# Kernel tuning notes

Hardware: AMD Instinct MI355X
Metric: run time of the kernel (lower is better)

The kernel has to match this reference:

```python
import jax, jax.numpy as jnp
import numpy as np

N = 100000   # nodes
E = 800000   # edges
F = 64       # num_features == hidden_dim
D = 64       # hidden_dim
L = 3        # num_gc_layers
NG = 512     # num graphs in batch
BN_EPS = 1e-5


def setup_inputs() -> dict:
    key = jax.random.key(0)
    ks = jax.random.split(key, 16)
    s = 0.05
    return {
        "x": jax.random.normal(ks[0], (N, F), jnp.float32),
        "edge_index": jax.random.randint(ks[1], (2, E), 0, N),
        "batch": jnp.sort(jax.random.randint(ks[2], (N,), 0, NG)),
        "W1": jax.random.normal(ks[3], (L, F, D), jnp.float32) * s,
        "b1": jnp.zeros((L, D), jnp.float32),
        "W2": jax.random.normal(ks[4], (L, D, D), jnp.float32) * s,
        "b2": jnp.zeros((L, D), jnp.float32),
        "gin_eps": jnp.zeros((L,), jnp.float32),
        "gin_bias": jnp.zeros((L, D), jnp.float32),
        "bn_gamma": jnp.ones((L, D), jnp.float32),
        "bn_beta": jnp.zeros((L, D), jnp.float32),
        "Wp1": jax.random.normal(ks[5], (L * D, L * D), jnp.float32) * s,
        "bp1": jnp.zeros((L * D,), jnp.float32),
        "Wp2": jax.random.normal(ks[6], (L * D, L * D), jnp.float32) * s,
        "bp2": jnp.zeros((L * D,), jnp.float32),
    }


def reference(x, edge_index, batch, W1, b1, W2, b2, gin_eps, gin_bias,
              bn_gamma, bn_beta, Wp1, bp1, Wp2, bp2):
    row, col = edge_index[0], edge_index[1]
    h = x
    xs = []
    for i in range(L):
        # sparse adj @ h : sum over incoming edges (adj[row, col] = 1)
        agg = jax.ops.segment_sum(h[col], row, num_segments=N)
        z = (1.0 + gin_eps[i]) * h + agg
        # GIN internal MLP: Linear -> ReLU -> Linear -> ReLU
        z = jax.nn.relu(z @ W1[i] + b1[i])
        z = jax.nn.relu(z @ W2[i] + b2[i])
        # conv bias + relu (outer F.relu in Encoder is idempotent)
        z = jax.nn.relu(z + gin_bias[i])
        # BatchNorm1d, training mode: batch stats over nodes, biased variance
        mean = jnp.mean(z, axis=0)
        var = jnp.mean(jnp.square(z - mean), axis=0)
        h = (z - mean) * jax.lax.rsqrt(var + BN_EPS) * bn_gamma[i] + bn_beta[i]
        xs.append(h)
    # per-layer global add pool over graphs, then concat -> [NG, L*D]
    pooled = jnp.concatenate(
        [jax.ops.segment_sum(xi, batch, num_segments=NG) for xi in xs], axis=1)
    # projection head: Linear -> ReLU -> Linear
    y = jax.nn.relu(pooled @ Wp1 + bp1) @ Wp2 + bp2
    return y
```

## Files before the change

kernel.cpp:

```cpp
#include <hip/hip_runtime.h>

#define N_NODES 100000
#define N_EDGES 800000
#define DF 64
#define NGRAPH 512
#define LDIM 192
#define BN_EPS 1e-5
#define NTILES 6250
#define GIN_GRID 1563
#define NWT (GIN_GRID * 4)
#define COLS_CAP 2600000
#define NBUCK 782
#define BCAP 2048
#define NBLK 128
#define CHUNK 6250

typedef __attribute__((ext_vector_type(8))) short bf16x8;
typedef __attribute__((ext_vector_type(4))) float f32x4;

__device__ inline short f2bf(float x) {
    union { float f; unsigned u; } v; v.f = x;
    unsigned r = v.u + 0x7fff + ((v.u >> 16) & 1);
    return (short)(r >> 16);
}

__device__ inline int pdeg_of(int d) {
    int p = (d + 15) & ~15;
    return p < 16 ? 16 : p;
}

__global__ __launch_bounds__(256) void blk_hist_kernel(
    const int* __restrict__ ei, int* __restrict__ hist)
{
    __shared__ int hh[NBUCK];
    int blk = blockIdx.x, tid = threadIdx.x;
    for (int i = tid; i < NBUCK; i += 256) hh[i] = 0;
    __syncthreads();
    int start = blk * CHUNK, end = min(start + CHUNK, N_EDGES);
    for (int e = start + tid; e < end; e += 256)
        atomicAdd(&hh[ei[e] >> 7], 1);
    __syncthreads();
    for (int i = tid; i < NBUCK; i += 256) hist[blk * NBUCK + i] = hh[i];
}

__global__ __launch_bounds__(NBLK) void blk_scan_kernel(
    const int* __restrict__ hist, int* __restrict__ pos, int* __restrict__ cnt)
{
    __shared__ int buf[NBLK];
    int k = blockIdx.x, b = threadIdx.x;
    int v = hist[b * NBUCK + k];
    buf[b] = v;
    __syncthreads();
    for (int o = 1; o < NBLK; o <<= 1) {
        int t = (b >= o) ? buf[b - o] : 0;
        __syncthreads();
        buf[b] += t;
        __syncthreads();
    }
    pos[b * NBUCK + k] = buf[b] - v;
    if (b == NBLK - 1) cnt[k] = buf[b];
}

__global__ __launch_bounds__(256) void place_kernel(
    const int* __restrict__ ei, const int* __restrict__ pos,
    unsigned* __restrict__ bucketData)
{
    __shared__ int cursor[NBUCK];
    int blk = blockIdx.x, tid = threadIdx.x;
    for (int i = tid; i < NBUCK; i += 256) cursor[i] = pos[blk * NBUCK + i];
    __syncthreads();
    int start = blk * CHUNK, end = min(start + CHUNK, N_EDGES);
    for (int e = start + tid; e < end; e += 256) {
        int r = ei[e];
        int c = ei[N_EDGES + e];
        int k = r >> 7;
        int p = atomicAdd(&cursor[k], 1);
        bucketData[(size_t)k * BCAP + p] = ((unsigned)(r & 127) << 17) | (unsigned)c;
    }
}

__global__ __launch_bounds__(256) void bucket_count_kernel(
    const unsigned* __restrict__ bucketData, const int* __restrict__ cnt,
    int* __restrict__ deg, int* __restrict__ bpad)
{
    __shared__ int rc[128];
    __shared__ int red[4];
    int b = blockIdx.x, tid = threadIdx.x;
    int rowbase = b << 7;
    int nrows = min(128, N_NODES - rowbase);
    int cntb = cnt[b];
    if (tid < 128) rc[tid] = 0;
    __syncthreads();
    for (int e = tid; e < cntb; e += 256)
        atomicAdd(&rc[bucketData[(size_t)b * BCAP + e] >> 17], 1);
    __syncthreads();
    int v = 0;
    if (tid < nrows) {
        int d = rc[tid];
        deg[rowbase + tid] = d;
        v = pdeg_of(d);
    }
    #pragma unroll
    for (int o = 32; o > 0; o >>= 1) v += __shfl_down(v, o, 64);
    if ((tid & 63) == 0) red[tid >> 6] = v;
    __syncthreads();
    if (tid == 0) bpad[b] = red[0] + red[1] + red[2] + red[3];
}

__global__ __launch_bounds__(1024) void bucket_scan_kernel(
    const int* __restrict__ bpad, int* __restrict__ bbase)
{
    __shared__ int buf[1024];
    int tid = threadIdx.x;
    int own = (tid < NBUCK) ? bpad[tid] : 0;
    buf[tid] = own;
    __syncthreads();
    for (int o = 1; o < 1024; o <<= 1) {
        int t = (tid >= o) ? buf[tid - o] : 0;
        __syncthreads();
        buf[tid] += t;
        __syncthreads();
    }
    if (tid < NBUCK) bbase[tid] = buf[tid] - own;
}

__global__ __launch_bounds__(256) void bucket_emit_kernel(
    const unsigned* __restrict__ bucketData, const int* __restrict__ cnt,
    const int* __restrict__ bbase,
    int* __restrict__ off, int* __restrict__ colS)
{
    __shared__ int rc[128], rstart[128], rcur[128], sbuf[128];
    __shared__ int region[4096];
    int b = blockIdx.x, tid = threadIdx.x;
    int rowbase = b << 7;
    int nrows = min(128, N_NODES - rowbase);
    int cntb = cnt[b];
    int base = bbase[b];
    if (tid < 128) rc[tid] = 0;
    __syncthreads();
    for (int e = tid; e < cntb; e += 256)
        atomicAdd(&rc[bucketData[(size_t)b * BCAP + e] >> 17], 1);
    __syncthreads();
    int pd = (tid < nrows) ? pdeg_of(rc[tid]) : 0;
    if (tid < 128) sbuf[tid] = pd;
    __syncthreads();
    for (int o = 1; o < 128; o <<= 1) {
        int t = 0;
        if (tid < 128 && tid >= o) t = sbuf[tid - o];
        __syncthreads();
        if (tid < 128) sbuf[tid] += t;
        __syncthreads();
    }
    if (tid < 128) { rstart[tid] = sbuf[tid] - pd; rcur[tid] = sbuf[tid] - pd; }
    __syncthreads();
    int total = sbuf[127];
    for (int e = tid; e < cntb; e += 256) {
        unsigned p = bucketData[(size_t)b * BCAP + e];
        int lr = p >> 17;
        int c = p & 0x1FFFF;
        int pos = atomicAdd(&rcur[lr], 1);
        region[pos] = c * DF;
    }
    __syncthreads();
    for (int i = tid; i < nrows; i += 256) {
        int st = rstart[i] + rc[i];
        int en = rstart[i] + pdeg_of(rc[i]);
        int sent = (rowbase + i) * DF;
        for (int j = st; j < en; ++j) region[j] = sent;
    }
    __syncthreads();
    for (int k = tid; k < total; k += 256) colS[base + k] = region[k];
    if (tid < nrows) off[rowbase + tid] = base + rstart[tid];
    if (b == NBUCK - 1 && tid == 0) off[N_NODES] = base + total;
}

__global__ __launch_bounds__(256) void gstart_kernel(
    const int* __restrict__ batch, int* __restrict__ gstart)
{
    int g = blockIdx.x * 256 + threadIdx.x;
    if (g > NGRAPH) return;
    if (g == NGRAPH) { gstart[g] = N_NODES; return; }
    int lo = 0, hi = N_NODES;
    while (lo < hi) {
        int mid = (lo + hi) >> 1;
        if (batch[mid] < g) lo = mid + 1; else hi = mid;
    }
    gstart[g] = lo;
}

__global__ void init_id_kernel(float* __restrict__ idsc, float* __restrict__ idsh)
{
    int f = threadIdx.x;
    idsc[f] = 1.0f;
    idsh[f] = 0.0f;
}

__global__ __launch_bounds__(256) void pack_w_kernel(
    const float* __restrict__ W1, const float* __restrict__ W2,
    short* __restrict__ Wpk)
{
    int u = blockIdx.x;
    int layer = u >> 1, gm = u & 1;
    const float* W = (gm ? W2 : W1) + layer * 4096;
    short* dst = Wpk + u * 4096;
    for (int idx = threadIdx.x; idx < 4096; idx += 256) {
        int i = idx & 7;
        int l = (idx >> 3) & 63;
        int rest = idx >> 9;
        int kt = rest & 1, nt = rest >> 1;
        int k = kt * 32 + (l >> 4) * 8 + i;
        int n = nt * 16 + (l & 15);
        dst[idx] = f2bf(W[k * 64 + n]);
    }
}

__global__ __launch_bounds__(256) void gin_layer_kernel(
    const float* __restrict__ zp,
    const float* __restrict__ sc_in,
    const float* __restrict__ sh_in,
    const int* __restrict__ off,
    const int* __restrict__ deg,
    const int* __restrict__ colS,
    float* __restrict__ zout,
    const short* __restrict__ Wpk,
    const float* __restrict__ b1,
    const float* __restrict__ b2,
    const float* __restrict__ gin_eps,
    const float* __restrict__ gin_bias,
    float* __restrict__ part_s,
    float* __restrict__ part_q)
{
    __shared__ __align__(16) short Wp1s[4096];
    __shared__ __align__(16) short Wp2s[4096];
    __shared__ __align__(16) short zs[4][16 * 72];

    int tid = threadIdx.x;
    {
        const short4* s1 = (const short4*)Wpk;
        const short4* s2 = (const short4*)(Wpk + 4096);
        short4* d1 = (short4*)Wp1s;
        short4* d2 = (short4*)Wp2s;
        for (int i = tid; i < 1024; i += 256) { d1[i] = s1[i]; d2[i] = s2[i]; }
    }

    int w = tid >> 6, l = tid & 63;
    int lr = l & 15;
    int lk = l >> 4;
    float epsf = 1.0f + gin_eps[0];
    float scf = sc_in[l], shf = sh_in[l];
    float b1f[4], b2f[4], gbf[4];
    #pragma unroll
    for (int nt = 0; nt < 4; ++nt) {
        b1f[nt] = b1[nt * 16 + lr];
        b2f[nt] = b2[nt * 16 + lr];
        gbf[nt] = gin_bias[nt * 16 + lr];
    }
    float ssum[4] = {0, 0, 0, 0}, sq[4] = {0, 0, 0, 0};
    short* zw = zs[w];
    __syncthreads();

    int t = blockIdx.x * 4 + w;
    bool active = t < NTILES;
    int n0 = t * 16;

    if (active) {
        #pragma unroll 1
        for (int mp = 0; mp < 8; ++mp) {
            int nodeA = n0 + (mp << 1);
            int nodeB = nodeA + 1;
            int sA = __builtin_amdgcn_readfirstlane(off[nodeA]);
            int eA = __builtin_amdgcn_readfirstlane(off[nodeA + 1]);
            int dA = __builtin_amdgcn_readfirstlane(deg[nodeA]);
            int sB = __builtin_amdgcn_readfirstlane(off[nodeB]);
            int eB = __builtin_amdgcn_readfirstlane(off[nodeB + 1]);
            int dB = __builtin_amdgcn_readfirstlane(deg[nodeB]);
            float hnA = zp[nodeA * DF + l];
            float hnB = zp[nodeB * DF + l];
            float vA[16], vB[16];
            #pragma unroll
            for (int j = 0; j < 16; ++j) {
                int co = __builtin_amdgcn_readfirstlane(colS[sA + j]);
                vA[j] = zp[co + l];
            }
            #pragma unroll
            for (int j = 0; j < 16; ++j) {
                int co = __builtin_amdgcn_readfirstlane(colS[sB + j]);
                vB[j] = zp[co + l];
            }
            float aA0 = (vA[0] + vA[1]) + (vA[2] + vA[3]);
            float aA1 = (vA[4] + vA[5]) + (vA[6] + vA[7]);
            float aA2 = (vA[8] + vA[9]) + (vA[10] + vA[11]);
            float aA3 = (vA[12] + vA[13]) + (vA[14] + vA[15]);
            float accA = (aA0 + aA1) + (aA2 + aA3);
            float aB0 = (vB[0] + vB[1]) + (vB[2] + vB[3]);
            float aB1 = (vB[4] + vB[5]) + (vB[6] + vB[7]);
            float aB2 = (vB[8] + vB[9]) + (vB[10] + vB[11]);
            float aB3 = (vB[12] + vB[13]) + (vB[14] + vB[15]);
            float accB = (aB0 + aB1) + (aB2 + aB3);
            for (int i = sA + 16; i < eA; i += 16) {
                #pragma unroll
                for (int j = 0; j < 16; ++j) {
                    int co = __builtin_amdgcn_readfirstlane(colS[i + j]);
                    accA += zp[co + l];
                }
            }
            for (int i = sB + 16; i < eB; i += 16) {
                #pragma unroll
                for (int j = 0; j < 16; ++j) {
                    int co = __builtin_amdgcn_readfirstlane(colS[i + j]);
                    accB += zp[co + l];
                }
            }
            float npA = (float)(eA - sA - dA);
            float npB = (float)(eB - sB - dB);
            float zfA = scf * ((epsf - npA) * hnA + accA) + (epsf + (float)dA) * shf;
            float zfB = scf * ((epsf - npB) * hnB + accB) + (epsf + (float)dB) * shf;
            zw[(mp * 2) * 72 + l] = f2bf(zfA);
            zw[(mp * 2 + 1) * 72 + l] = f2bf(zfB);
        }

        {
            bf16x8 a0 = *(const bf16x8*)&zw[lr * 72 + lk * 8];
            bf16x8 a1 = *(const bf16x8*)&zw[lr * 72 + 32 + lk * 8];
            #pragma unroll
            for (int nt = 0; nt < 4; ++nt) {
                f32x4 acc = {0.f, 0.f, 0.f, 0.f};
                bf16x8 bb0 = *(const bf16x8*)&Wp1s[((nt * 2 + 0) * 64 + l) * 8];
                bf16x8 bb1 = *(const bf16x8*)&Wp1s[((nt * 2 + 1) * 64 + l) * 8];
                acc = __builtin_amdgcn_mfma_f32_16x16x32_bf16(a0, bb0, acc, 0, 0, 0);
                acc = __builtin_amdgcn_mfma_f32_16x16x32_bf16(a1, bb1, acc, 0, 0, 0);
                #pragma unroll
                for (int r = 0; r < 4; ++r) {
                    float v = fmaxf(acc[r] + b1f[nt], 0.0f);
                    zw[(lk * 4 + r) * 72 + nt * 16 + lr] = f2bf(v);
                }
            }
        }

        {
            bf16x8 a0 = *(const bf16x8*)&zw[lr * 72 + lk * 8];
            bf16x8 a1 = *(const bf16x8*)&zw[lr * 72 + 32 + lk * 8];
            #pragma unroll
            for (int nt = 0; nt < 4; ++nt) {
                f32x4 acc = {0.f, 0.f, 0.f, 0.f};
                bf16x8 bb0 = *(const bf16x8*)&Wp2s[((nt * 2 + 0) * 64 + l) * 8];
                bf16x8 bb1 = *(const bf16x8*)&Wp2s[((nt * 2 + 1) * 64 + l) * 8];
                acc = __builtin_amdgcn_mfma_f32_16x16x32_bf16(a0, bb0, acc, 0, 0, 0);
                acc = __builtin_amdgcn_mfma_f32_16x16x32_bf16(a1, bb1, acc, 0, 0, 0);
                #pragma unroll
                for (int r = 0; r < 4; ++r) {
                    float v = fmaxf(fmaxf(acc[r] + b2f[nt], 0.0f) + gbf[nt], 0.0f);
                    zout[(n0 + lk * 4 + r) * DF + nt * 16 + lr] = v;
                    ssum[nt] += v;
                    sq[nt] += v * v;
                }
            }
        }
    }

    #pragma unroll
    for (int nt = 0; nt < 4; ++nt) {
        float sv = ssum[nt], qv = sq[nt];
        sv += __shfl_xor(sv, 16, 64); sv += __shfl_xor(sv, 32, 64);
        qv += __shfl_xor(qv, 16, 64); qv += __shfl_xor(qv, 32, 64);
        if (l < 16) {
            part_s[(nt * 16 + l) * NWT + t] = sv;
            part_q[(nt * 16 + l) * NWT + t] = qv;
        }
    }
}

__global__ __launch_bounds__(256) void stat_reduce_kernel(
    const float* __restrict__ part_s, const float* __restrict__ part_q,
    const float* __restrict__ gamma, const float* __restrict__ beta,
    float* __restrict__ scale, float* __restrict__ shift)
{
    __shared__ double rs[4], rq[4];
    int f = blockIdx.x, tid = threadIdx.x;
    double s = 0.0, q = 0.0;
    for (int j = tid; j < NWT; j += 256) {
        s += (double)part_s[f * NWT + j];
        q += (double)part_q[f * NWT + j];
    }
    for (int o = 32; o > 0; o >>= 1) {
        s += __shfl_down(s, o, 64);
        q += __shfl_down(q, o, 64);
    }
    if ((tid & 63) == 0) { rs[tid >> 6] = s; rq[tid >> 6] = q; }
    __syncthreads();
    if (tid == 0) {
        double st = rs[0] + rs[1] + rs[2] + rs[3];
        double qt = rq[0] + rq[1] + rq[2] + rq[3];
        double mean = st / N_NODES;
        double var = qt / N_NODES - mean * mean;
        double inv = (double)gamma[f] / sqrt(var + BN_EPS);
        scale[f] = (float)inv;
        shift[f] = (float)((double)beta[f] - mean * inv);
    }
}

__global__ __launch_bounds__(256) void pool_kernel(
    const float* __restrict__ z,
    const float* __restrict__ scale,
    const float* __restrict__ shift,
    const int* __restrict__ gstart,
    float* __restrict__ pooled,
    int layerOff)
{
    __shared__ float red[4][64];
    int g = blockIdx.x;
    int tid = threadIdx.x;
    int w = tid >> 6, f = tid & 63;

    int s = gstart[g], e = gstart[g + 1];
    float acc = 0.0f;
    for (int node = s + w; node < e; node += 4)
        acc += z[node * DF + f];
    red[w][f] = acc;
    __syncthreads();
    if (w == 0)
        pooled[g * LDIM + layerOff + f] =
            scale[f] * (red[0][f] + red[1][f] + red[2][f] + red[3][f])
            + (float)(e - s) * shift[f];
}

__global__ __launch_bounds__(192) void proj_kernel(
    const float* __restrict__ in,
    const float* __restrict__ W,
    const float* __restrict__ b,
    float* __restrict__ out,
    int do_relu)
{
    __shared__ float rowS[LDIM];
    int r = blockIdx.x;
    int c = threadIdx.x;
    rowS[c] = in[r * LDIM + c];
    __syncthreads();
    float acc = b[c];
    #pragma unroll 4
    for (int k = 0; k < LDIM; ++k) acc += rowS[k] * W[k * LDIM + c];
    out[r * LDIM + c] = do_relu ? fmaxf(acc, 0.0f) : acc;
}

extern "C" void kernel_launch(void* const* d_in, const int* in_sizes, int n_in,
                              void* d_out, int out_size, void* d_ws, size_t ws_size,
                              hipStream_t stream)
{
    const float* x        = (const float*)d_in[0];
    const int*   ei       = (const int*)d_in[1];
    const int*   batch    = (const int*)d_in[2];
    const float* W1       = (const float*)d_in[3];
    const float* b1       = (const float*)d_in[4];
    const float* W2       = (const float*)d_in[5];
    const float* b2       = (const float*)d_in[6];
    const float* gin_eps  = (const float*)d_in[7];
    const float* gin_bias = (const float*)d_in[8];
    const float* gamma    = (const float*)d_in[9];
    const float* beta     = (const float*)d_in[10];
    const float* Wp1      = (const float*)d_in[11];
    const float* bp1      = (const float*)d_in[12];
    const float* Wp2      = (const float*)d_in[13];
    const float* bp2      = (const float*)d_in[14];
    float* out = (float*)d_out;

    float* bufA = (float*)d_ws;
    float* bufB = bufA + (size_t)N_NODES * DF;
    float* pooled = bufB + (size_t)N_NODES * DF;
    float* hidden = pooled + (size_t)NGRAPH * LDIM;
    float* scale = hidden + (size_t)NGRAPH * LDIM;
    float* shift = scale + 64;
    float* idsc = shift + 64;
    float* idsh = idsc + 64;
    float* part_s = idsh + 64;
    float* part_q = part_s + (size_t)64 * NWT;
    int* gstart = (int*)(part_q + (size_t)64 * NWT);
    int* deg  = gstart + NGRAPH + 1;
    int* off  = deg + N_NODES;
    int* colS = off + N_NODES + 1;
    int* hist = colS + COLS_CAP;
    int* pos  = hist + NBLK * NBUCK;
    int* cnt  = pos + NBLK * NBUCK;
    int* bpad = cnt + NBUCK;
    int* bbase = bpad + NBUCK;
    unsigned* bucketData = (unsigned*)(bbase + NBUCK);
    short* Wpk = (short*)(bucketData + (size_t)NBUCK * BCAP);

    blk_hist_kernel<<<NBLK, 256, 0, stream>>>(ei, hist);
    blk_scan_kernel<<<NBUCK, NBLK, 0, stream>>>(hist, pos, cnt);
    place_kernel<<<NBLK, 256, 0, stream>>>(ei, pos, bucketData);
    bucket_count_kernel<<<NBUCK, 256, 0, stream>>>(bucketData, cnt, deg, bpad);
    bucket_scan_kernel<<<1, 1024, 0, stream>>>(bpad, bbase);
    bucket_emit_kernel<<<NBUCK, 256, 0, stream>>>(bucketData, cnt, bbase,
                                                  off, colS);
    gstart_kernel<<<3, 256, 0, stream>>>(batch, gstart);
    init_id_kernel<<<1, 64, 0, stream>>>(idsc, idsh);
    pack_w_kernel<<<6, 256, 0, stream>>>(W1, W2, Wpk);

    const float* zprev = x;
    const float* sc_in = idsc;
    const float* sh_in = idsh;
    float* zbuf[2] = {bufA, bufB};
    for (int l = 0; l < 3; ++l) {
        float* zcur = zbuf[l & 1];
        gin_layer_kernel<<<GIN_GRID, 256, 0, stream>>>(
            zprev, sc_in, sh_in, off, deg, colS, zcur,
            Wpk + (size_t)l * 8192,
            b1 + l * 64, b2 + l * 64, gin_eps + l, gin_bias + l * 64,
            part_s, part_q);

        stat_reduce_kernel<<<64, 256, 0, stream>>>(
            part_s, part_q, gamma + l * 64, beta + l * 64, scale, shift);

        pool_kernel<<<NGRAPH, 256, 0, stream>>>(
            zcur, scale, shift, gstart, pooled, l * 64);

        zprev = zcur;
        sc_in = scale;
        sh_in = shift;
    }

    proj_kernel<<<NGRAPH, LDIM, 0, stream>>>(pooled, Wp1, bp1, hidden, 1);
    proj_kernel<<<NGRAPH, LDIM, 0, stream>>>(hidden, Wp2, bp2, out, 0);
}
```

Measured before the change: 294.2 us.

## Store intermediate node features in bf16 and fuse projection kernels

```diff
diff --git a/kernel.cpp b/kernel.cpp
--- a/kernel.cpp
+++ b/kernel.cpp
@@ -24,6 +24,12 @@
     return (short)(r >> 16);
 }
 
+__device__ inline float bf2f(unsigned short u) {
+    union { unsigned u; float f; } v;
+    v.u = ((unsigned)u) << 16;
+    return v.f;
+}
+
 __device__ inline int pdeg_of(int d) {
     int p = (d + 15) & ~15;
     return p < 16 ? 16 : p;
@@ -175,9 +181,11 @@
 }
 
 __global__ __launch_bounds__(256) void gstart_kernel(
-    const int* __restrict__ batch, int* __restrict__ gstart)
+    const int* __restrict__ batch, int* __restrict__ gstart,
+    float* __restrict__ idsc, float* __restrict__ idsh)
 {
     int g = blockIdx.x * 256 + threadIdx.x;
+    if (g < 64) { idsc[g] = 1.0f; idsh[g] = 0.0f; }
     if (g > NGRAPH) return;
     if (g == NGRAPH) { gstart[g] = N_NODES; return; }
     int lo = 0, hi = N_NODES;
@@ -186,13 +194,6 @@
         if (batch[mid] < g) lo = mid + 1; else hi = mid;
     }
     gstart[g] = lo;
-}
-
-__global__ void init_id_kernel(float* __restrict__ idsc, float* __restrict__ idsh)
-{
-    int f = threadIdx.x;
-    idsc[f] = 1.0f;
-    idsh[f] = 0.0f;
 }
 
 __global__ __launch_bounds__(256) void pack_w_kernel(
@@ -214,14 +215,15 @@
     }
 }
 
+template <bool BF16IN>
 __global__ __launch_bounds__(256) void gin_layer_kernel(
-    const float* __restrict__ zp,
+    const void* __restrict__ zp_,
     const float* __restrict__ sc_in,
     const float* __restrict__ sh_in,
     const int* __restrict__ off,
     const int* __restrict__ deg,
     const int* __restrict__ colS,
-    float* __restrict__ zout,
+    unsigned short* __restrict__ zout,
     const short* __restrict__ Wpk,
     const float* __restrict__ b1,
     const float* __restrict__ b2,
@@ -233,6 +235,9 @@
     __shared__ __align__(16) short Wp1s[4096];
     __shared__ __align__(16) short Wp2s[4096];
     __shared__ __align__(16) short zs[4][16 * 72];
+
+    const float* zpf = (const float*)zp_;
+    const unsigned short* zpb = (const unsigned short*)zp_;
 
     int tid = threadIdx.x;
     {
@@ -274,18 +279,19 @@
             int sB = __builtin_amdgcn_readfirstlane(off[nodeB]);
             int eB = __builtin_amdgcn_readfirstlane(off[nodeB + 1]);
             int dB = __builtin_amdgcn_readfirstlane(deg[nodeB]);
-            float hnA = zp[nodeA * DF + l];
-            float hnB = zp[nodeB * DF + l];
+            float hnA, hnB;
+            if (BF16IN) { hnA = bf2f(zpb[nodeA * DF + l]); hnB = bf2f(zpb[nodeB * DF + l]); }
+            else        { hnA = zpf[nodeA * DF + l];       hnB = zpf[nodeB * DF + l]; }
             float vA[16], vB[16];
             #pragma unroll
             for (int j = 0; j < 16; ++j) {
                 int co = __builtin_amdgcn_readfirstlane(colS[sA + j]);
-                vA[j] = zp[co + l];
+                vA[j] = BF16IN ? bf2f(zpb[co + l]) : zpf[co + l];
             }
             #pragma unroll
             for (int j = 0; j < 16; ++j) {
                 int co = __builtin_amdgcn_readfirstlane(colS[sB + j]);
-                vB[j] = zp[co + l];
+                vB[j] = BF16IN ? bf2f(zpb[co + l]) : zpf[co + l];
             }
             float aA0 = (vA[0] + vA[1]) + (vA[2] + vA[3]);
             float aA1 = (vA[4] + vA[5]) + (vA[6] + vA[7]);
@@ -301,14 +307,14 @@
                 #pragma unroll
                 for (int j = 0; j < 16; ++j) {
                     int co = __builtin_amdgcn_readfirstlane(colS[i + j]);
-                    accA += zp[co + l];
+                    accA += BF16IN ? bf2f(zpb[co + l]) : zpf[co + l];
                 }
             }
             for (int i = sB + 16; i < eB; i += 16) {
                 #pragma unroll
                 for (int j = 0; j < 16; ++j) {
                     int co = __builtin_amdgcn_readfirstlane(colS[i + j]);
-                    accB += zp[co + l];
+                    accB += BF16IN ? bf2f(zpb[co + l]) : zpf[co + l];
                 }
             }
             float npA = (float)(eA - sA - dA);
@@ -350,9 +356,11 @@
                 #pragma unroll
                 for (int r = 0; r < 4; ++r) {
                     float v = fmaxf(fmaxf(acc[r] + b2f[nt], 0.0f) + gbf[nt], 0.0f);
-                    zout[(n0 + lk * 4 + r) * DF + nt * 16 + lr] = v;
-                    ssum[nt] += v;
-                    sq[nt] += v * v;
+                    unsigned short vb = (unsigned short)f2bf(v);
+                    zout[(n0 + lk * 4 + r) * DF + nt * 16 + lr] = vb;
+                    float vr = bf2f(vb);
+                    ssum[nt] += vr;
+                    sq[nt] += vr * vr;
                 }
             }
         }
@@ -400,7 +408,7 @@
 }
 
 __global__ __launch_bounds__(256) void pool_kernel(
-    const float* __restrict__ z,
+    const unsigned short* __restrict__ z,
     const float* __restrict__ scale,
     const float* __restrict__ shift,
     const int* __restrict__ gstart,
@@ -415,7 +423,7 @@
     int s = gstart[g], e = gstart[g + 1];
     float acc = 0.0f;
     for (int node = s + w; node < e; node += 4)
-        acc += z[node * DF + f];
+        acc += bf2f(z[node * DF + f]);
     red[w][f] = acc;
     __syncthreads();
     if (w == 0)
@@ -424,22 +432,27 @@
             + (float)(e - s) * shift[f];
 }
 
-__global__ __launch_bounds__(192) void proj_kernel(
+__global__ __launch_bounds__(192) void proj_fused_kernel(
     const float* __restrict__ in,
-    const float* __restrict__ W,
-    const float* __restrict__ b,
-    float* __restrict__ out,
-    int do_relu)
+    const float* __restrict__ Wp1, const float* __restrict__ bp1,
+    const float* __restrict__ Wp2, const float* __restrict__ bp2,
+    float* __restrict__ out)
 {
     __shared__ float rowS[LDIM];
+    __shared__ float hid[LDIM];
     int r = blockIdx.x;
     int c = threadIdx.x;
     rowS[c] = in[r * LDIM + c];
     __syncthreads();
-    float acc = b[c];
+    float acc = bp1[c];
     #pragma unroll 4
-    for (int k = 0; k < LDIM; ++k) acc += rowS[k] * W[k * LDIM + c];
-    out[r * LDIM + c] = do_relu ? fmaxf(acc, 0.0f) : acc;
+    for (int k = 0; k < LDIM; ++k) acc += rowS[k] * Wp1[k * LDIM + c];
+    hid[c] = fmaxf(acc, 0.0f);
+    __syncthreads();
+    float acc2 = bp2[c];
+    #pragma unroll 4
+    for (int k = 0; k < LDIM; ++k) acc2 += hid[k] * Wp2[k * LDIM + c];
+    out[r * LDIM + c] = acc2;
 }
 
 extern "C" void kernel_launch(void* const* d_in, const int* in_sizes, int n_in,
@@ -463,11 +476,10 @@
     const float* bp2      = (const float*)d_in[14];
     float* out = (float*)d_out;
 
-    float* bufA = (float*)d_ws;
-    float* bufB = bufA + (size_t)N_NODES * DF;
-    float* pooled = bufB + (size_t)N_NODES * DF;
-    float* hidden = pooled + (size_t)NGRAPH * LDIM;
-    float* scale = hidden + (size_t)NGRAPH * LDIM;
+    unsigned short* zbufA = (unsigned short*)d_ws;
+    unsigned short* zbufB = zbufA + (size_t)N_NODES * DF;
+    float* pooled = (float*)(zbufB + (size_t)N_NODES * DF);
+    float* scale = pooled + (size_t)NGRAPH * LDIM;
     float* shift = scale + 64;
     float* idsc = shift + 64;
     float* idsh = idsc + 64;
@@ -492,21 +504,27 @@
     bucket_scan_kernel<<<1, 1024, 0, stream>>>(bpad, bbase);
     bucket_emit_kernel<<<NBUCK, 256, 0, stream>>>(bucketData, cnt, bbase,
                                                   off, colS);
-    gstart_kernel<<<3, 256, 0, stream>>>(batch, gstart);
-    init_id_kernel<<<1, 64, 0, stream>>>(idsc, idsh);
+    gstart_kernel<<<3, 256, 0, stream>>>(batch, gstart, idsc, idsh);
     pack_w_kernel<<<6, 256, 0, stream>>>(W1, W2, Wpk);
 
-    const float* zprev = x;
+    unsigned short* zbuf[2] = {zbufA, zbufB};
+    const void* zprev = (const void*)x;
     const float* sc_in = idsc;
     const float* sh_in = idsh;
-    float* zbuf[2] = {bufA, bufB};
     for (int l = 0; l < 3; ++l) {
-        float* zcur = zbuf[l & 1];
-        gin_layer_kernel<<<GIN_GRID, 256, 0, stream>>>(
-            zprev, sc_in, sh_in, off, deg, colS, zcur,
-            Wpk + (size_t)l * 8192,
-            b1 + l * 64, b2 + l * 64, gin_eps + l, gin_bias + l * 64,
-            part_s, part_q);
+        unsigned short* zcur = zbuf[l & 1];
+        if (l == 0)
+            gin_layer_kernel<false><<<GIN_GRID, 256, 0, stream>>>(
+                zprev, sc_in, sh_in, off, deg, colS, zcur,
+                Wpk + (size_t)l * 8192,
+                b1 + l * 64, b2 + l * 64, gin_eps + l, gin_bias + l * 64,
+                part_s, part_q);
+        else
+            gin_layer_kernel<true><<<GIN_GRID, 256, 0, stream>>>(
+                zprev, sc_in, sh_in, off, deg, colS, zcur,
+                Wpk + (size_t)l * 8192,
+                b1 + l * 64, b2 + l * 64, gin_eps + l, gin_bias + l * 64,
+                part_s, part_q);
 
         stat_reduce_kernel<<<64, 256, 0, stream>>>(
             part_s, part_q, gamma + l * 64, beta + l * 64, scale, shift);
@@ -514,11 +532,10 @@
         pool_kernel<<<NGRAPH, 256, 0, stream>>>(
             zcur, scale, shift, gstart, pooled, l * 64);
 
-        zprev = zcur;
+        zprev = (const void*)zcur;
         sc_in = scale;
         sh_in = shift;
     }
 
-    proj_kernel<<<NGRAPH, LDIM, 0, stream>>>(pooled, Wp1, bp1, hidden, 1);
-    proj_kernel<<<NGRAPH, LDIM, 0, stream>>>(hidden, Wp2, bp2, out, 0);
-}
+    proj_fused_kernel<<<NGRAPH, LDIM, 0, stream>>>(pooled, Wp1, bp1, Wp2, bp2, out);
+}
```

After: 278.0 us. 1.06x faster.
